# Optimization experiments

Hardware: AMD Instinct MI355X
Metric: run time of the kernel (lower is better)

The kernel has to match this reference:

```python
import jax, jax.numpy as jnp
import numpy as np

G = 8          # group (window) size -> N = G*G = 64
HEADS = 8
DIM = 256
HEAD_DIM = DIM // HEADS
SCALE = HEAD_DIM ** -0.5
POS_DIM = (DIM // 4) // 4  # 16
LN_EPS = 1e-5


def _make_bias_tables():
    # biases: coordinates (1-g..g-1) x (1-g..g-1) -> [(2g-1)^2, 2] float
    r = np.arange(1 - G, G)
    bh, bw = np.meshgrid(r, r, indexing='ij')
    biases = np.stack([bh.ravel(), bw.ravel()], axis=1).astype(np.float32)
    # relative position index [g^2, g^2]
    ch, cw = np.meshgrid(np.arange(G), np.arange(G), indexing='ij')
    coords = np.stack([ch.ravel(), cw.ravel()])              # [2, g^2]
    rel = coords[:, :, None] - coords[:, None, :]            # [2, g^2, g^2]
    rel = rel.transpose(1, 2, 0)
    rel[:, :, 0] += G - 1
    rel[:, :, 1] += G - 1
    rel[:, :, 0] *= 2 * G - 1
    rel_idx = rel.sum(-1).astype(np.int32)                   # [g^2, g^2]
    return biases, rel_idx


def setup_inputs() -> dict:
    key = jax.random.key(0)
    ks = jax.random.split(key, 8)
    B, N, C = 2048, G * G, DIM
    biases_np, rel_idx_np = _make_bias_tables()
    s = lambda fan: 1.0 / np.sqrt(fan)
    return {
        'x': jax.random.normal(ks[0], (B, N, C), jnp.float32),
        'qkv_w': jax.random.normal(ks[1], (C, 3 * C), jnp.float32) * s(C),
        'qkv_b': jnp.zeros((3 * C,), jnp.float32),
        'proj_w': jax.random.normal(ks[2], (C, C), jnp.float32) * s(C),
        'proj_b': jnp.zeros((C,), jnp.float32),
        'pos_proj_w': jax.random.normal(ks[3], (2, POS_DIM), jnp.float32) * s(2),
        'pos_proj_b': jnp.zeros((POS_DIM,), jnp.float32),
        'ln1_g': jnp.ones((POS_DIM,), jnp.float32), 'ln1_b': jnp.zeros((POS_DIM,), jnp.float32),
        'fc1_w': jax.random.normal(ks[4], (POS_DIM, POS_DIM), jnp.float32) * s(POS_DIM),
        'fc1_b': jnp.zeros((POS_DIM,), jnp.float32),
        'ln2_g': jnp.ones((POS_DIM,), jnp.float32), 'ln2_b': jnp.zeros((POS_DIM,), jnp.float32),
        'fc2_w': jax.random.normal(ks[5], (POS_DIM, POS_DIM), jnp.float32) * s(POS_DIM),
        'fc2_b': jnp.zeros((POS_DIM,), jnp.float32),
        'ln3_g': jnp.ones((POS_DIM,), jnp.float32), 'ln3_b': jnp.zeros((POS_DIM,), jnp.float32),
        'fc3_w': jax.random.normal(ks[6], (POS_DIM, HEADS), jnp.float32) * s(POS_DIM),
        'fc3_b': jnp.zeros((HEADS,), jnp.float32),
        'biases': jnp.asarray(biases_np),
        'rel_idx': jnp.asarray(rel_idx_np),
    }


def _ln(h, g, b):
    m = jnp.mean(h, -1, keepdims=True)
    v = jnp.mean((h - m) ** 2, -1, keepdims=True)
    return (h - m) * jax.lax.rsqrt(v + LN_EPS) * g + b


def reference(x, qkv_w, qkv_b, proj_w, proj_b,
              pos_proj_w, pos_proj_b,
              ln1_g, ln1_b, fc1_w, fc1_b,
              ln2_g, ln2_b, fc2_w, fc2_b,
              ln3_g, ln3_b, fc3_w, fc3_b,
              biases, rel_idx):
    B, N, C = x.shape
    # dynamic position bias MLP: [(2g-1)^2, 2] -> [(2g-1)^2, heads]
    h = biases @ pos_proj_w + pos_proj_b
    h = jax.nn.relu(_ln(h, ln1_g, ln1_b)) @ fc1_w + fc1_b
    h = jax.nn.relu(_ln(h, ln2_g, ln2_b)) @ fc2_w + fc2_b
    pos = jax.nn.relu(_ln(h, ln3_g, ln3_b)) @ fc3_w + fc3_b        # [225, H]
    rel_bias = pos[rel_idx]                                        # [N, N, H]
    rel_bias = jnp.transpose(rel_bias, (2, 0, 1))                  # [H, N, N]

    qkv = (x @ qkv_w + qkv_b).reshape(B, N, 3, HEADS, HEAD_DIM)
    qkv = jnp.transpose(qkv, (2, 0, 3, 1, 4))                      # [3, B, H, N, Dh]
    q, k, v = qkv[0] * SCALE, qkv[1], qkv[2]
    attn = jnp.einsum('bhnd,bhmd->bhnm', q, k) + rel_bias[None]    # [B, H, N, N]
    attn = jax.nn.softmax(attn, axis=-1)
    out = jnp.einsum('bhnm,bhmd->bhnd', attn, v)                   # [B, H, N, Dh]
    out = jnp.transpose(out, (0, 2, 1, 3)).reshape(B, N, C)
    return out @ proj_w + proj_b
```

## Files before the change

kernel.cpp:

```cpp
#include <hip/hip_runtime.h>

typedef _Float16 half_t;
typedef __attribute__((ext_vector_type(8))) _Float16 half8;
typedef __attribute__((ext_vector_type(4))) _Float16 half4;
typedef __attribute__((ext_vector_type(4))) float float4v;

#define LN_EPS 1e-5f
#define QK_SCALE 0.17677669529663687f

static __device__ __forceinline__ float4v mfma16(half8 a, half8 b, float4v c) {
    return __builtin_amdgcn_mfma_f32_16x16x32_f16(a, b, c, 0, 0, 0);
}

static __device__ __forceinline__ int swzA(int row, int colByte) {
    return row * 512 + ((((colByte >> 4) ^ ((row >> 1) & 7)) << 4) | (colByte & 15));
}
static __device__ __forceinline__ int swzB(int row, int colByte) {
    return row * 64 + ((((colByte >> 4) ^ ((row >> 1) & 3)) << 4) | (colByte & 15));
}

static __device__ void ln_relu16(float* h, const float* __restrict__ g, const float* __restrict__ b) {
    float m = 0.f;
    for (int j = 0; j < 16; ++j) m += h[j];
    m *= (1.0f / 16.0f);
    float v = 0.f;
    for (int j = 0; j < 16; ++j) { float d = h[j] - m; v += d * d; }
    v *= (1.0f / 16.0f);
    float rs = rsqrtf(v + LN_EPS);
    for (int j = 0; j < 16; ++j) {
        float t = (h[j] - m) * rs * g[j] + b[j];
        h[j] = t > 0.f ? t : 0.f;
    }
}

__global__ void prep_kernel(
    const float* __restrict__ qkv_w,
    const float* __restrict__ proj_w,
    const float* __restrict__ biases,
    const float* __restrict__ pos_w, const float* __restrict__ pos_b,
    const float* __restrict__ ln1_g, const float* __restrict__ ln1_b,
    const float* __restrict__ fc1_w, const float* __restrict__ fc1_b,
    const float* __restrict__ ln2_g, const float* __restrict__ ln2_b,
    const float* __restrict__ fc2_w, const float* __restrict__ fc2_b,
    const float* __restrict__ ln3_g, const float* __restrict__ ln3_b,
    const float* __restrict__ fc3_w, const float* __restrict__ fc3_b,
    const int* __restrict__ rel_idx,
    half_t* __restrict__ wqkvT,
    half_t* __restrict__ wprojT,
    float* __restrict__ rbp)
{
    __shared__ float tile[64][65];
    __shared__ float pos_s[225][8];
    const int t = blockIdx.x;
    const int tid = threadIdx.x;

    if (t < 64) {
        const float* src; half_t* dst; int ncols, rg, cg;
        if (t < 48) { src = qkv_w;  dst = wqkvT;  ncols = 768; rg = t / 12;      cg = t % 12; }
        else        { src = proj_w; dst = wprojT; ncols = 256; rg = (t-48) >> 2; cg = (t-48) & 3; }
        const int r0 = tid >> 6, c = tid & 63;
        for (int i = 0; i < 16; ++i) {
            int r = i * 4 + r0;
            tile[r][c] = src[(rg * 64 + r) * ncols + cg * 64 + c];
        }
        __syncthreads();
        for (int i = 0; i < 16; ++i) {
            int r = i * 4 + r0;
            dst[(cg * 64 + r) * 256 + rg * 64 + c] = (half_t)tile[c][r];
        }
    } else {
        if (tid < 225) {
            float h[16], h2[16];
            float b0 = biases[tid * 2], b1 = biases[tid * 2 + 1];
            for (int j = 0; j < 16; ++j) h[j] = b0 * pos_w[j] + b1 * pos_w[16 + j] + pos_b[j];
            ln_relu16(h, ln1_g, ln1_b);
            for (int j = 0; j < 16; ++j) {
                float s = fc1_b[j];
                for (int k = 0; k < 16; ++k) s += h[k] * fc1_w[k * 16 + j];
                h2[j] = s;
            }
            ln_relu16(h2, ln2_g, ln2_b);
            for (int j = 0; j < 16; ++j) {
                float s = fc2_b[j];
                for (int k = 0; k < 16; ++k) s += h2[k] * fc2_w[k * 16 + j];
                h[j] = s;
            }
            ln_relu16(h, ln3_g, ln3_b);
            for (int j = 0; j < 8; ++j) {
                float s = fc3_b[j];
                for (int k = 0; k < 16; ++k) s += h[k] * fc3_w[k * 8 + j];
                pos_s[tid][j] = s;
            }
        }
        __syncthreads();
        for (int e = tid; e < 8 * 64 * 64; e += 256) {
            int hh = e >> 12, rem = e & 4095;
            int row = rem >> 6, c = rem & 63;
            int tj = c >> 4, mm = c & 15;
            rbp[hh * 4096 + row * 64 + mm * 4 + tj] = pos_s[rel_idx[row * 64 + c]][hh];
        }
    }
}

__global__ __launch_bounds__(512, 2) void fused_kernel(
    const float* __restrict__ x,
    const half_t* __restrict__ wqkvT,
    const float* __restrict__ qkv_b,
    const half_t* __restrict__ wprojT,
    const float* __restrict__ proj_b,
    const float* __restrict__ rbp,
    float* __restrict__ out)
{
    __shared__ __align__(16) char smem[81920];
    char* xs  = smem;
    char* atn = smem;
    char* arenas = smem + 32768;

    const int b   = blockIdx.x;
    const int tid = threadIdx.x;
    const int w    = tid >> 6;
    const int lane = tid & 63;
    const int m = lane & 15;
    const int g = lane >> 4;
    char* wA = arenas + w * 6144;
    char* wB = arenas + w * 6144 + 4096;

    const float* xg = x + (size_t)b * 16384;
    #pragma unroll
    for (int i = 0; i < 8; ++i) {
        int u = tid + i * 512;
        int row = u >> 6, c4 = u & 63;
        float4v xv = *(const float4v*)(xg + u * 4);
        half4 hv;
        hv[0] = (half_t)xv[0]; hv[1] = (half_t)xv[1];
        hv[2] = (half_t)xv[2]; hv[3] = (half_t)xv[3];
        *(half4*)(xs + swzA(row, c4 * 8)) = hv;
    }
    __syncthreads();

    half8 aq[4], bk[4];
    #pragma unroll
    for (int pt = 0; pt < 2; ++pt) {
        const int wrow0 = pt * 256 + w * 32;
        #pragma unroll
        for (int c2 = 0; c2 < 2; ++c2) {
            float4v a4[4];
            #pragma unroll
            for (int ti = 0; ti < 4; ++ti) a4[ti] = {0.f, 0.f, 0.f, 0.f};
            #pragma unroll
            for (int kk = 0; kk < 8; ++kk) {
                half8 wf = *(const half8*)(wqkvT + (size_t)(wrow0 + c2 * 16 + m) * 256 + kk * 32 + g * 8);
                #pragma unroll
                for (int ti = 0; ti < 4; ++ti) {
                    half8 af = *(const half8*)(xs + swzA(ti * 16 + m, kk * 64 + g * 16));
                    a4[ti] = mfma16(wf, af, a4[ti]);
                }
            }
            float4v b4 = *(const float4v*)(qkv_b + wrow0 + c2 * 16 + g * 4);
            #pragma unroll
            for (int ti = 0; ti < 4; ++ti) {
                half4 t;
                #pragma unroll
                for (int r = 0; r < 4; ++r) t[r] = (half_t)(a4[ti][r] + b4[r]);
                *(half4*)(wA + ti * 1024 + swzB(m, (c2 * 16 + g * 4) * 2)) = t;
            }
        }
        #pragma unroll
        for (int ti = 0; ti < 4; ++ti) {
            half8 fr = *(const half8*)(wA + ti * 1024 + swzB(m, g * 16));
            if (pt == 0) aq[ti] = fr; else bk[ti] = fr;
        }
        __builtin_amdgcn_sched_barrier(0);
    }

    half4 ph[4][4];
    const float* rbh = rbp + w * 4096;
    #pragma unroll
    for (int ti = 0; ti < 4; ++ti) {
        float4v z = {0.f, 0.f, 0.f, 0.f};
        float4v s0 = mfma16(aq[ti], bk[0], z);
        float4v s1 = mfma16(aq[ti], bk[1], z);
        float4v s2 = mfma16(aq[ti], bk[2], z);
        float4v s3 = mfma16(aq[ti], bk[3], z);
        #pragma unroll
        for (int r = 0; r < 4; ++r) {
            float4v rb = *(const float4v*)(rbh + (ti * 16 + g * 4 + r) * 64 + m * 4);
            float e0 = __expf(s0[r] * QK_SCALE + rb[0]);
            float e1 = __expf(s1[r] * QK_SCALE + rb[1]);
            float e2 = __expf(s2[r] * QK_SCALE + rb[2]);
            float e3 = __expf(s3[r] * QK_SCALE + rb[3]);
            float s = e0 + e1 + e2 + e3;
            s += __shfl_xor(s, 1); s += __shfl_xor(s, 2);
            s += __shfl_xor(s, 4); s += __shfl_xor(s, 8);
            float is = 1.0f / s;
            ph[ti][0][r] = (half_t)(e0 * is);
            ph[ti][1][r] = (half_t)(e1 * is);
            ph[ti][2][r] = (half_t)(e2 * is);
            ph[ti][3][r] = (half_t)(e3 * is);
        }
    }

    half4 vh[2][4];
    #pragma unroll
    for (int c2 = 0; c2 < 2; ++c2) {
        const int wrow0 = 512 + w * 32;
        float4v a4[4];
        #pragma unroll
        for (int ti = 0; ti < 4; ++ti) a4[ti] = {0.f, 0.f, 0.f, 0.f};
        #pragma unroll
        for (int kk = 0; kk < 8; ++kk) {
            half8 wf = *(const half8*)(wqkvT + (size_t)(wrow0 + c2 * 16 + m) * 256 + kk * 32 + g * 8);
            #pragma unroll
            for (int ti = 0; ti < 4; ++ti) {
                half8 af = *(const half8*)(xs + swzA(ti * 16 + m, kk * 64 + g * 16));
                a4[ti] = mfma16(af, wf, a4[ti]);
            }
        }
        float vb = qkv_b[wrow0 + c2 * 16 + m];
        #pragma unroll
        for (int ti = 0; ti < 4; ++ti)
            #pragma unroll
            for (int r = 0; r < 4; ++r)
                vh[c2][ti][r] = (half_t)(a4[ti][r] + vb);
    }
    __syncthreads();

    #pragma unroll
    for (int tjd = 0; tjd < 2; ++tjd) {
        float4v o4[4];
        #pragma unroll
        for (int ti = 0; ti < 4; ++ti) o4[ti] = {0.f, 0.f, 0.f, 0.f};
        #pragma unroll
        for (int nc = 0; nc < 2; ++nc) {
            #pragma unroll
            for (int ti = 0; ti < 4; ++ti)
                #pragma unroll
                for (int t2 = 0; t2 < 2; ++t2)
                    #pragma unroll
                    for (int r = 0; r < 4; ++r)
                        *(half_t*)(wA + swzB(ti * 16 + g * 4 + r, (t2 * 16 + m) * 2)) =
                            ph[ti][nc * 2 + t2][r];
            #pragma unroll
            for (int t2 = 0; t2 < 2; ++t2)
                *(half4*)(wB + swzB(m, (t2 * 16 + g * 4) * 2)) = vh[tjd][nc * 2 + t2];
            half8 bv = *(const half8*)(wB + swzB(m, g * 16));
            #pragma unroll
            for (int ti = 0; ti < 4; ++ti) {
                half8 pa = *(const half8*)(wA + swzB(ti * 16 + m, g * 16));
                o4[ti] = mfma16(pa, bv, o4[ti]);
            }
            __builtin_amdgcn_sched_barrier(0);
        }
        #pragma unroll
        for (int ti = 0; ti < 4; ++ti)
            #pragma unroll
            for (int r = 0; r < 4; ++r)
                *(half_t*)(atn + swzA(ti * 16 + g * 4 + r, (w * 32 + tjd * 16 + m) * 2)) =
                    (half_t)o4[ti][r];
    }
    __syncthreads();

    float* og = out + (size_t)b * 16384;
    const int oc0 = w * 32;
    float4v pacc[2][4];
    #pragma unroll
    for (int c2 = 0; c2 < 2; ++c2)
        #pragma unroll
        for (int ti = 0; ti < 4; ++ti) pacc[c2][ti] = {0.f, 0.f, 0.f, 0.f};
    #pragma unroll
    for (int kk = 0; kk < 8; ++kk) {
        half8 wf0 = *(const half8*)(wprojT + (size_t)(oc0 +      m) * 256 + kk * 32 + g * 8);
        half8 wf1 = *(const half8*)(wprojT + (size_t)(oc0 + 16 + m) * 256 + kk * 32 + g * 8);
        #pragma unroll
        for (int ti = 0; ti < 4; ++ti) {
            half8 af = *(const half8*)(atn + swzA(ti * 16 + m, kk * 64 + g * 16));
            pacc[0][ti] = mfma16(af, wf0, pacc[0][ti]);
            pacc[1][ti] = mfma16(af, wf1, pacc[1][ti]);
        }
    }
    float pb0 = proj_b[oc0 + m], pb1 = proj_b[oc0 + 16 + m];
    #pragma unroll
    for (int c2 = 0; c2 < 2; ++c2)
        #pragma unroll
        for (int ti = 0; ti < 4; ++ti)
            #pragma unroll
            for (int r = 0; r < 4; ++r)
                og[(ti * 16 + g * 4 + r) * 256 + oc0 + c2 * 16 + m] =
                    pacc[c2][ti][r] + (c2 ? pb1 : pb0);
}

extern "C" void kernel_launch(void* const* d_in, const int* in_sizes, int n_in,
                              void* d_out, int out_size, void* d_ws, size_t ws_size,
                              hipStream_t stream) {
    const float* x          = (const float*)d_in[0];
    const float* qkv_w      = (const float*)d_in[1];
    const float* qkv_b      = (const float*)d_in[2];
    const float* proj_w     = (const float*)d_in[3];
    const float* proj_b     = (const float*)d_in[4];
    const float* pos_proj_w = (const float*)d_in[5];
    const float* pos_proj_b = (const float*)d_in[6];
    const float* ln1_g = (const float*)d_in[7];
    const float* ln1_b = (const float*)d_in[8];
    const float* fc1_w = (const float*)d_in[9];
    const float* fc1_b = (const float*)d_in[10];
    const float* ln2_g = (const float*)d_in[11];
    const float* ln2_b = (const float*)d_in[12];
    const float* fc2_w = (const float*)d_in[13];
    const float* fc2_b = (const float*)d_in[14];
    const float* ln3_g = (const float*)d_in[15];
    const float* ln3_b = (const float*)d_in[16];
    const float* fc3_w = (const float*)d_in[17];
    const float* fc3_b = (const float*)d_in[18];
    const float* biases = (const float*)d_in[19];
    const int*  rel_idx = (const int*)d_in[20];

    half_t* wqkvT  = (half_t*)d_ws;
    half_t* wprojT = (half_t*)((char*)d_ws + 393216);
    float*  rbp    = (float*)((char*)d_ws + 524288);

    const int B = in_sizes[0] / (64 * 256);

    prep_kernel<<<65, 256, 0, stream>>>(qkv_w, proj_w, biases, pos_proj_w, pos_proj_b,
                                        ln1_g, ln1_b, fc1_w, fc1_b,
                                        ln2_g, ln2_b, fc2_w, fc2_b,
                                        ln3_g, ln3_b, fc3_w, fc3_b,
                                        rel_idx, wqkvT, wprojT, rbp);
    fused_kernel<<<B, 512, 0, stream>>>(x, wqkvT, qkv_b, wprojT, proj_b, rbp,
                                        (float*)d_out);
}
```

Baseline: 258.1 us.

## Recompute softmax probabilities per chunk to cut registers and LDS for higher occupancy

Instead of holding the normalized fp16 probabilities for all 64 columns in registers, the kernel keeps only the per-row reciprocal sums and recomputes the QK scores and exponentials chunk by chunk just before the PV MMA. V is now staged once per warp in the freed x-tile region with a new swizzle, so the per-warp arena shrinks and total LDS drops from 80KB to 64KB. Launch bounds go from 2 to 4 blocks per SM, and the projection loop is split so fewer accumulators are live at once. The cost is redundant QK MFMAs, a second pass of exps and bias loads, and an extra block barrier.

```diff
diff --git a/kernel.cpp b/kernel.cpp
--- a/kernel.cpp
+++ b/kernel.cpp
@@ -17,6 +17,9 @@
 }
 static __device__ __forceinline__ int swzB(int row, int colByte) {
     return row * 64 + ((((colByte >> 4) ^ ((row >> 1) & 3)) << 4) | (colByte & 15));
+}
+static __device__ __forceinline__ int swzC(int row, int colByte) {
+    return row * 128 + ((((colByte >> 4) ^ (row & 7)) << 4) | (colByte & 15));
 }
 
 static __device__ void ln_relu16(float* h, const float* __restrict__ g, const float* __restrict__ b) {
@@ -102,7 +105,7 @@
     }
 }
 
-__global__ __launch_bounds__(512, 2) void fused_kernel(
+__global__ __launch_bounds__(512, 4) void fused_kernel(
     const float* __restrict__ x,
     const half_t* __restrict__ wqkvT,
     const float* __restrict__ qkv_b,
@@ -111,7 +114,7 @@
     const float* __restrict__ rbp,
     float* __restrict__ out)
 {
-    __shared__ __align__(16) char smem[81920];
+    __shared__ __align__(16) char smem[65536];
     char* xs  = smem;
     char* atn = smem;
     char* arenas = smem + 32768;
@@ -122,8 +125,8 @@
     const int lane = tid & 63;
     const int m = lane & 15;
     const int g = lane >> 4;
-    char* wA = arenas + w * 6144;
-    char* wB = arenas + w * 6144 + 4096;
+    char* wA  = arenas + w * 4096;
+    char* vts = xs + w * 4096;
 
     const float* xg = x + (size_t)b * 16384;
     #pragma unroll
@@ -173,7 +176,7 @@
         __builtin_amdgcn_sched_barrier(0);
     }
 
-    half4 ph[4][4];
+    float rinv[4][4];
     const float* rbh = rbp + w * 4096;
     #pragma unroll
     for (int ti = 0; ti < 4; ++ti) {
@@ -192,11 +195,7 @@
             float s = e0 + e1 + e2 + e3;
             s += __shfl_xor(s, 1); s += __shfl_xor(s, 2);
             s += __shfl_xor(s, 4); s += __shfl_xor(s, 8);
-            float is = 1.0f / s;
-            ph[ti][0][r] = (half_t)(e0 * is);
-            ph[ti][1][r] = (half_t)(e1 * is);
-            ph[ti][2][r] = (half_t)(e2 * is);
-            ph[ti][3][r] = (half_t)(e3 * is);
+            rinv[ti][r] = 1.0f / s;
         }
     }
 
@@ -226,67 +225,79 @@
     __syncthreads();
 
     #pragma unroll
-    for (int tjd = 0; tjd < 2; ++tjd) {
-        float4v o4[4];
-        #pragma unroll
-        for (int ti = 0; ti < 4; ++ti) o4[ti] = {0.f, 0.f, 0.f, 0.f};
-        #pragma unroll
-        for (int nc = 0; nc < 2; ++nc) {
-            #pragma unroll
-            for (int ti = 0; ti < 4; ++ti)
-                #pragma unroll
-                for (int t2 = 0; t2 < 2; ++t2)
-                    #pragma unroll
-                    for (int r = 0; r < 4; ++r)
-                        *(half_t*)(wA + swzB(ti * 16 + g * 4 + r, (t2 * 16 + m) * 2)) =
-                            ph[ti][nc * 2 + t2][r];
-            #pragma unroll
-            for (int t2 = 0; t2 < 2; ++t2)
-                *(half4*)(wB + swzB(m, (t2 * 16 + g * 4) * 2)) = vh[tjd][nc * 2 + t2];
-            half8 bv = *(const half8*)(wB + swzB(m, g * 16));
+    for (int c2 = 0; c2 < 2; ++c2)
+        #pragma unroll
+        for (int ti = 0; ti < 4; ++ti)
+            *(half4*)(vts + swzC(c2 * 16 + m, ti * 32 + g * 8)) = vh[c2][ti];
+
+    float4v oacc[2][4];
+    #pragma unroll
+    for (int tjd = 0; tjd < 2; ++tjd)
+        #pragma unroll
+        for (int ti = 0; ti < 4; ++ti) oacc[tjd][ti] = {0.f, 0.f, 0.f, 0.f};
+    #pragma unroll
+    for (int nc = 0; nc < 2; ++nc) {
+        #pragma unroll
+        for (int ti = 0; ti < 4; ++ti) {
+            float4v z = {0.f, 0.f, 0.f, 0.f};
+            float4v sa = mfma16(aq[ti], bk[2 * nc], z);
+            float4v sb = mfma16(aq[ti], bk[2 * nc + 1], z);
+            #pragma unroll
+            for (int r = 0; r < 4; ++r) {
+                int row = ti * 16 + g * 4 + r;
+                float4v rb = *(const float4v*)(rbh + row * 64 + m * 4);
+                float pa_ = __expf(sa[r] * QK_SCALE + rb[2 * nc])     * rinv[ti][r];
+                float pb_ = __expf(sb[r] * QK_SCALE + rb[2 * nc + 1]) * rinv[ti][r];
+                *(half_t*)(wA + swzB(row, m * 2))      = (half_t)pa_;
+                *(half_t*)(wA + swzB(row, 32 + m * 2)) = (half_t)pb_;
+            }
+        }
+        #pragma unroll
+        for (int tjd = 0; tjd < 2; ++tjd) {
+            half8 bv = *(const half8*)(vts + swzC(tjd * 16 + m, nc * 64 + g * 16));
             #pragma unroll
             for (int ti = 0; ti < 4; ++ti) {
                 half8 pa = *(const half8*)(wA + swzB(ti * 16 + m, g * 16));
-                o4[ti] = mfma16(pa, bv, o4[ti]);
-            }
-            __builtin_amdgcn_sched_barrier(0);
-        }
+                oacc[tjd][ti] = mfma16(pa, bv, oacc[tjd][ti]);
+            }
+        }
+        __builtin_amdgcn_sched_barrier(0);
+    }
+    __syncthreads();
+
+    #pragma unroll
+    for (int tjd = 0; tjd < 2; ++tjd)
         #pragma unroll
         for (int ti = 0; ti < 4; ++ti)
             #pragma unroll
             for (int r = 0; r < 4; ++r)
                 *(half_t*)(atn + swzA(ti * 16 + g * 4 + r, (w * 32 + tjd * 16 + m) * 2)) =
-                    (half_t)o4[ti][r];
-    }
+                    (half_t)oacc[tjd][ti][r];
     __syncthreads();
 
     float* og = out + (size_t)b * 16384;
     const int oc0 = w * 32;
-    float4v pacc[2][4];
-    #pragma unroll
-    for (int c2 = 0; c2 < 2; ++c2)
-        #pragma unroll
-        for (int ti = 0; ti < 4; ++ti) pacc[c2][ti] = {0.f, 0.f, 0.f, 0.f};
-    #pragma unroll
-    for (int kk = 0; kk < 8; ++kk) {
-        half8 wf0 = *(const half8*)(wprojT + (size_t)(oc0 +      m) * 256 + kk * 32 + g * 8);
-        half8 wf1 = *(const half8*)(wprojT + (size_t)(oc0 + 16 + m) * 256 + kk * 32 + g * 8);
-        #pragma unroll
-        for (int ti = 0; ti < 4; ++ti) {
-            half8 af = *(const half8*)(atn + swzA(ti * 16 + m, kk * 64 + g * 16));
-            pacc[0][ti] = mfma16(af, wf0, pacc[0][ti]);
-            pacc[1][ti] = mfma16(af, wf1, pacc[1][ti]);
-        }
-    }
-    float pb0 = proj_b[oc0 + m], pb1 = proj_b[oc0 + 16 + m];
-    #pragma unroll
-    for (int c2 = 0; c2 < 2; ++c2)
+    #pragma unroll
+    for (int c2 = 0; c2 < 2; ++c2) {
+        float4v p4[4];
+        #pragma unroll
+        for (int ti = 0; ti < 4; ++ti) p4[ti] = {0.f, 0.f, 0.f, 0.f};
+        #pragma unroll
+        for (int kk = 0; kk < 8; ++kk) {
+            half8 wf = *(const half8*)(wprojT + (size_t)(oc0 + c2 * 16 + m) * 256 + kk * 32 + g * 8);
+            #pragma unroll
+            for (int ti = 0; ti < 4; ++ti) {
+                half8 af = *(const half8*)(atn + swzA(ti * 16 + m, kk * 64 + g * 16));
+                p4[ti] = mfma16(af, wf, p4[ti]);
+            }
+        }
+        float pb = proj_b[oc0 + c2 * 16 + m];
         #pragma unroll
         for (int ti = 0; ti < 4; ++ti)
             #pragma unroll
             for (int r = 0; r < 4; ++r)
-                og[(ti * 16 + g * 4 + r) * 256 + oc0 + c2 * 16 + m] =
-                    pacc[c2][ti][r] + (c2 ? pb1 : pb0);
+                og[(ti * 16 + g * 4 + r) * 256 + oc0 + c2 * 16 + m] = p4[ti][r] + pb;
+    }
 }
 
 extern "C" void kernel_launch(void* const* d_in, const int* in_sizes, int n_in,
```

After: 581.3 us. +125.2%, slower.

## Halve block to 4 waves, each processing two heads, shrink LDS arenas

Applied to the files above, without the earlier changes.

The fused attention kernel now launches 256 threads per window, and each wave handles two heads in sequence instead of one. Per-wave LDS scratch shrinks, so total shared memory per block drops from 80KB to 52KB, allowing more blocks per CU (launch bounds changed to 256,3). The PV stage is reordered so P fragments are loaded once and reused across both V column tiles, and the projection loop now runs four 16-column tiles per wave. Per-head outputs are held in registers across the loop, which raises register pressure. There is also less intra-block parallelism per window.

```diff
diff --git a/kernel.cpp b/kernel.cpp
--- a/kernel.cpp
+++ b/kernel.cpp
@@ -102,7 +102,7 @@
     }
 }
 
-__global__ __launch_bounds__(512, 2) void fused_kernel(
+__global__ __launch_bounds__(256, 3) void fused_kernel(
     const float* __restrict__ x,
     const half_t* __restrict__ wqkvT,
     const float* __restrict__ qkv_b,
@@ -111,10 +111,9 @@
     const float* __restrict__ rbp,
     float* __restrict__ out)
 {
-    __shared__ __align__(16) char smem[81920];
+    __shared__ __align__(16) char smem[53248];
     char* xs  = smem;
     char* atn = smem;
-    char* arenas = smem + 32768;
 
     const int b   = blockIdx.x;
     const int tid = threadIdx.x;
@@ -122,13 +121,13 @@
     const int lane = tid & 63;
     const int m = lane & 15;
     const int g = lane >> 4;
-    char* wA = arenas + w * 6144;
-    char* wB = arenas + w * 6144 + 4096;
+    char* wA = smem + 32768 + w * 5120;
+    char* wB = wA + 4096;
 
     const float* xg = x + (size_t)b * 16384;
     #pragma unroll
-    for (int i = 0; i < 8; ++i) {
-        int u = tid + i * 512;
+    for (int i = 0; i < 16; ++i) {
+        int u = tid + i * 256;
         int row = u >> 6, c4 = u & 63;
         float4v xv = *(const float4v*)(xg + u * 4);
         half4 hv;
@@ -138,12 +137,78 @@
     }
     __syncthreads();
 
-    half8 aq[4], bk[4];
+    half4 oh[2][2][4];
+
     #pragma unroll
-    for (int pt = 0; pt < 2; ++pt) {
-        const int wrow0 = pt * 256 + w * 32;
+    for (int hh = 0; hh < 2; ++hh) {
+        const int h = w + hh * 4;
+        const float* rbh = rbp + h * 4096;
+
+        half8 aq[4], bk[4];
+        #pragma unroll
+        for (int pt = 0; pt < 2; ++pt) {
+            const int wrow0 = pt * 256 + h * 32;
+            #pragma unroll
+            for (int c2 = 0; c2 < 2; ++c2) {
+                float4v a4[4];
+                #pragma unroll
+                for (int ti = 0; ti < 4; ++ti) a4[ti] = {0.f, 0.f, 0.f, 0.f};
+                #pragma unroll
+                for (int kk = 0; kk < 8; ++kk) {
+                    half8 wf = *(const half8*)(wqkvT + (size_t)(wrow0 + c2 * 16 + m) * 256 + kk * 32 + g * 8);
+                    #pragma unroll
+                    for (int ti = 0; ti < 4; ++ti) {
+                        half8 af = *(const half8*)(xs + swzA(ti * 16 + m, kk * 64 + g * 16));
+                        a4[ti] = mfma16(wf, af, a4[ti]);
+                    }
+                }
+                float4v b4 = *(const float4v*)(qkv_b + wrow0 + c2 * 16 + g * 4);
+                #pragma unroll
+                for (int ti = 0; ti < 4; ++ti) {
+                    half4 t;
+                    #pragma unroll
+                    for (int r = 0; r < 4; ++r) t[r] = (half_t)(a4[ti][r] + b4[r]);
+                    *(half4*)(wA + ti * 1024 + swzB(m, (c2 * 16 + g * 4) * 2)) = t;
+                }
+            }
+            #pragma unroll
+            for (int ti = 0; ti < 4; ++ti) {
+                half8 fr = *(const half8*)(wA + ti * 1024 + swzB(m, g * 16));
+                if (pt == 0) aq[ti] = fr; else bk[ti] = fr;
+            }
+            __builtin_amdgcn_sched_barrier(0);
+        }
+
+        half4 ph[4][4];
+        #pragma unroll
+        for (int ti = 0; ti < 4; ++ti) {
+            float4v z = {0.f, 0.f, 0.f, 0.f};
+            float4v s0 = mfma16(aq[ti], bk[0], z);
+            float4v s1 = mfma16(aq[ti], bk[1], z);
+            float4v s2 = mfma16(aq[ti], bk[2], z);
+            float4v s3 = mfma16(aq[ti], bk[3], z);
+            #pragma unroll
+            for (int r = 0; r < 4; ++r) {
+                float4v rb = *(const float4v*)(rbh + (ti * 16 + g * 4 + r) * 64 + m * 4);
+                float e0 = __expf(s0[r] * QK_SCALE + rb[0]);
+                float e1 = __expf(s1[r] * QK_SCALE + rb[1]);
+                float e2 = __expf(s2[r] * QK_SCALE + rb[2]);
+                float e3 = __expf(s3[r] * QK_SCALE + rb[3]);
+                float s = e0 + e1 + e2 + e3;
+                s += __shfl_xor(s, 1); s += __shfl_xor(s, 2);
+                s += __shfl_xor(s, 4); s += __shfl_xor(s, 8);
+                float is = 1.0f / s;
+                ph[ti][0][r] = (half_t)(e0 * is);
+                ph[ti][1][r] = (half_t)(e1 * is);
+                ph[ti][2][r] = (half_t)(e2 * is);
+                ph[ti][3][r] = (half_t)(e3 * is);
+            }
+        }
+
+        half4 vh[2][4];
         #pragma unroll
         for (int c2 = 0; c2 < 2; ++c2) {
+            const int wrow0 = 512 + h * 32;
             float4v a4[4];
             #pragma unroll
             for (int ti = 0; ti < 4; ++ti) a4[ti] = {0.f, 0.f, 0.f, 0.f};
@@ -153,83 +218,22 @@
                 #pragma unroll
                 for (int ti = 0; ti < 4; ++ti) {
                     half8 af = *(const half8*)(xs + swzA(ti * 16 + m, kk * 64 + g * 16));
-                    a4[ti] = mfma16(wf, af, a4[ti]);
+                    a4[ti] = mfma16(af, wf, a4[ti]);
                 }
             }
-            float4v b4 = *(const float4v*)(qkv_b + wrow0 + c2 * 16 + g * 4);
-            #pragma unroll
-            for (int ti = 0; ti < 4; ++ti) {
-                half4 t;
-                #pragma unroll
-                for (int r = 0; r < 4; ++r) t[r] = (half_t)(a4[ti][r] + b4[r]);
-                *(half4*)(wA + ti * 1024 + swzB(m, (c2 * 16 + g * 4) * 2)) = t;
-            }
-        }
-        #pragma unroll
-        for (int ti = 0; ti < 4; ++ti) {
-            half8 fr = *(const half8*)(wA + ti * 1024 + swzB(m, g * 16));
-            if (pt == 0) aq[ti] = fr; else bk[ti] = fr;
-        }
-        __builtin_amdgcn_sched_barrier(0);
-    }
-
-    half4 ph[4][4];
-    const float* rbh = rbp + w * 4096;
-    #pragma unroll
-    for (int ti = 0; ti < 4; ++ti) {
-        float4v z = {0.f, 0.f, 0.f, 0.f};
-        float4v s0 = mfma16(aq[ti], bk[0], z);
-        float4v s1 = mfma16(aq[ti], bk[1], z);
-        float4v s2 = mfma16(aq[ti], bk[2], z);
-        float4v s3 = mfma16(aq[ti], bk[3], z);
-        #pragma unroll
-        for (int r = 0; r < 4; ++r) {
-            float4v rb = *(const float4v*)(rbh + (ti * 16 + g * 4 + r) * 64 + m * 4);
-            float e0 = __expf(s0[r] * QK_SCALE + rb[0]);
-            float e1 = __expf(s1[r] * QK_SCALE + rb[1]);
-            float e2 = __expf(s2[r] * QK_SCALE + rb[2]);
-            float e3 = __expf(s3[r] * QK_SCALE + rb[3]);
-            float s = e0 + e1 + e2 + e3;
-            s += __shfl_xor(s, 1); s += __shfl_xor(s, 2);
-            s += __shfl_xor(s, 4); s += __shfl_xor(s, 8);
-            float is = 1.0f / s;
-            ph[ti][0][r] = (half_t)(e0 * is);
-            ph[ti][1][r] = (half_t)(e1 * is);
-            ph[ti][2][r] = (half_t)(e2 * is);
-            ph[ti][3][r] = (half_t)(e3 * is);
-        }
-    }
-
-    half4 vh[2][4];
-    #pragma unroll
-    for (int c2 = 0; c2 < 2; ++c2) {
-        const int wrow0 = 512 + w * 32;
-        float4v a4[4];
-        #pragma unroll
-        for (int ti = 0; ti < 4; ++ti) a4[ti] = {0.f, 0.f, 0.f, 0.f};
-        #pragma unroll
-        for (int kk = 0; kk < 8; ++kk) {
-            half8 wf = *(const half8*)(wqkvT + (size_t)(wrow0 + c2 * 16 + m) * 256 + kk * 32 + g * 8);
-            #pragma unroll
-            for (int ti = 0; ti < 4; ++ti) {
-                half8 af = *(const half8*)(xs + swzA(ti * 16 + m, kk * 64 + g * 16));
-                a4[ti] = mfma16(af, wf, a4[ti]);
-            }
-        }
-        float vb = qkv_b[wrow0 + c2 * 16 + m];
-        #pragma unroll
-        for (int ti = 0; ti < 4; ++ti)
-            #pragma unroll
-            for (int r = 0; r < 4; ++r)
-                vh[c2][ti][r] = (half_t)(a4[ti][r] + vb);
-    }
-    __syncthreads();
-
-    #pragma unroll
-    for (int tjd = 0; tjd < 2; ++tjd) {
-        float4v o4[4];
-        #pragma unroll
-        for (int ti = 0; ti < 4; ++ti) o4[ti] = {0.f, 0.f, 0.f, 0.f};
+            float vb = qkv_b[wrow0 + c2 * 16 + m];
+            #pragma unroll
+            for (int ti = 0; ti < 4; ++ti)
+                #pragma unroll
+                for (int r = 0; r < 4; ++r)
+                    vh[c2][ti][r] = (half_t)(a4[ti][r] + vb);
+        }
+
+        float4v oacc[2][4];
+        #pragma unroll
+        for (int tjd = 0; tjd < 2; ++tjd)
+            #pragma unroll
+            for (int ti = 0; ti < 4; ++ti) oacc[tjd][ti] = {0.f, 0.f, 0.f, 0.f};
         #pragma unroll
         for (int nc = 0; nc < 2; ++nc) {
             #pragma unroll
@@ -240,53 +244,70 @@
                     for (int r = 0; r < 4; ++r)
                         *(half_t*)(wA + swzB(ti * 16 + g * 4 + r, (t2 * 16 + m) * 2)) =
                             ph[ti][nc * 2 + t2][r];
-            #pragma unroll
-            for (int t2 = 0; t2 < 2; ++t2)
-                *(half4*)(wB + swzB(m, (t2 * 16 + g * 4) * 2)) = vh[tjd][nc * 2 + t2];
-            half8 bv = *(const half8*)(wB + swzB(m, g * 16));
+            half8 pa[4];
+            #pragma unroll
+            for (int ti = 0; ti < 4; ++ti)
+                pa[ti] = *(const half8*)(wA + swzB(ti * 16 + m, g * 16));
+            __builtin_amdgcn_sched_barrier(0);
+            #pragma unroll
+            for (int tjd = 0; tjd < 2; ++tjd) {
+                #pragma unroll
+                for (int t2 = 0; t2 < 2; ++t2)
+                    *(half4*)(wB + swzB(m, (t2 * 16 + g * 4) * 2)) = vh[tjd][nc * 2 + t2];
+                half8 bv = *(const half8*)(wB + swzB(m, g * 16));
+                #pragma unroll
+                for (int ti = 0; ti < 4; ++ti)
+                    oacc[tjd][ti] = mfma16(pa[ti], bv, oacc[tjd][ti]);
+                __builtin_amdgcn_sched_barrier(0);
+            }
+        }
+        #pragma unroll
+        for (int tjd = 0; tjd < 2; ++tjd)
+            #pragma unroll
+            for (int ti = 0; ti < 4; ++ti)
+                #pragma unroll
+                for (int r = 0; r < 4; ++r)
+                    oh[hh][tjd][ti][r] = (half_t)oacc[tjd][ti][r];
+        __builtin_amdgcn_sched_barrier(0);
+    }
+    __syncthreads();
+
+    #pragma unroll
+    for (int hh = 0; hh < 2; ++hh)
+        #pragma unroll
+        for (int tjd = 0; tjd < 2; ++tjd)
+            #pragma unroll
+            for (int ti = 0; ti < 4; ++ti)
+                #pragma unroll
+                for (int r = 0; r < 4; ++r)
+                    *(half_t*)(atn + swzA(ti * 16 + g * 4 + r,
+                                          ((w + hh * 4) * 32 + tjd * 16 + m) * 2)) =
+                        oh[hh][tjd][ti][r];
+    __syncthreads();
+
+    float* og = out + (size_t)b * 16384;
+    #pragma unroll
+    for (int c4 = 0; c4 < 4; ++c4) {
+        const int oc0 = w * 64 + c4 * 16;
+        float4v p4[4];
+        #pragma unroll
+        for (int ti = 0; ti < 4; ++ti) p4[ti] = {0.f, 0.f, 0.f, 0.f};
+        #pragma unroll
+        for (int kk = 0; kk < 8; ++kk) {
+            half8 wf = *(const half8*)(wprojT + (size_t)(oc0 + m) * 256 + kk * 32 + g * 8);
             #pragma unroll
             for (int ti = 0; ti < 4; ++ti) {
-                half8 pa = *(const half8*)(wA + swzB(ti * 16 + m, g * 16));
-                o4[ti] = mfma16(pa, bv, o4[ti]);
-            }
-            __builtin_amdgcn_sched_barrier(0);
-        }
+                half8 af = *(const half8*)(atn + swzA(ti * 16 + m, kk * 64 + g * 16));
+                p4[ti] = mfma16(af, wf, p4[ti]);
+            }
+        }
+        float pb = proj_b[oc0 + m];
         #pragma unroll
         for (int ti = 0; ti < 4; ++ti)
             #pragma unroll
             for (int r = 0; r < 4; ++r)
-                *(half_t*)(atn + swzA(ti * 16 + g * 4 + r, (w * 32 + tjd * 16 + m) * 2)) =
-                    (half_t)o4[ti][r];
-    }
-    __syncthreads();
-
-    float* og = out + (size_t)b * 16384;
-    const int oc0 = w * 32;
-    float4v pacc[2][4];
-    #pragma unroll
-    for (int c2 = 0; c2 < 2; ++c2)
-        #pragma unroll
-        for (int ti = 0; ti < 4; ++ti) pacc[c2][ti] = {0.f, 0.f, 0.f, 0.f};
-    #pragma unroll
-    for (int kk = 0; kk < 8; ++kk) {
-        half8 wf0 = *(const half8*)(wprojT + (size_t)(oc0 +      m) * 256 + kk * 32 + g * 8);
-        half8 wf1 = *(const half8*)(wprojT + (size_t)(oc0 + 16 + m) * 256 + kk * 32 + g * 8);
-        #pragma unroll
-        for (int ti = 0; ti < 4; ++ti) {
-            half8 af = *(const half8*)(atn + swzA(ti * 16 + m, kk * 64 + g * 16));
-            pacc[0][ti] = mfma16(af, wf0, pacc[0][ti]);
-            pacc[1][ti] = mfma16(af, wf1, pacc[1][ti]);
-        }
-    }
-    float pb0 = proj_b[oc0 + m], pb1 = proj_b[oc0 + 16 + m];
-    #pragma unroll
-    for (int c2 = 0; c2 < 2; ++c2)
-        #pragma unroll
-        for (int ti = 0; ti < 4; ++ti)
-            #pragma unroll
-            for (int r = 0; r < 4; ++r)
-                og[(ti * 16 + g * 4 + r) * 256 + oc0 + c2 * 16 + m] =
-                    pacc[c2][ti][r] + (c2 ? pb1 : pb0);
+                og[(ti * 16 + g * 4 + r) * 256 + oc0 + m] = p4[ti][r] + pb;
+    }
 }
 
 extern "C" void kernel_launch(void* const* d_in, const int* in_sizes, int n_in,
@@ -325,6 +346,6 @@
                                         ln2_g, ln2_b, fc2_w, fc2_b,
                                         ln3_g, ln3_b, fc3_w, fc3_b,
                                         rel_idx, wqkvT, wprojT, rbp);
-    fused_kernel<<<B, 512, 0, stream>>>(x, wqkvT, qkv_b, wprojT, proj_b, rbp,
+    fused_kernel<<<B, 256, 0, stream>>>(x, wqkvT, qkv_b, wprojT, proj_b, rbp,
                                         (float*)d_out);
 }
```

Result: slower. 345.3 us (+33.8%).

## Fuse Q/K projection loops, stage V in shared memory, shrink LDS footprint

Applied to the files above, without the earlier changes.

Q and K projections are computed in a single k-loop so each x fragment read from LDS feeds four MFMA accumulators, and V columns are likewise computed together. V is written once into a swizzled per-wave region that reuses the x buffer, so the PV product no longer rewrites V for each output tile. The P fragments are loaded once and reused across both output column tiles. Shared memory drops from 80KB to 64KB, which may help occupancy, at the cost of more live accumulator registers and one extra block barrier.

```diff
diff --git a/kernel.cpp b/kernel.cpp
--- a/kernel.cpp
+++ b/kernel.cpp
@@ -17,6 +17,9 @@
 }
 static __device__ __forceinline__ int swzB(int row, int colByte) {
     return row * 64 + ((((colByte >> 4) ^ ((row >> 1) & 3)) << 4) | (colByte & 15));
+}
+static __device__ __forceinline__ int swzC(int row, int colByte) {
+    return row * 128 + ((((colByte >> 4) ^ (row & 7)) << 4) | (colByte & 15));
 }
 
 static __device__ void ln_relu16(float* h, const float* __restrict__ g, const float* __restrict__ b) {
@@ -111,7 +114,7 @@
     const float* __restrict__ rbp,
     float* __restrict__ out)
 {
-    __shared__ __align__(16) char smem[81920];
+    __shared__ __align__(16) char smem[65536];
     char* xs  = smem;
     char* atn = smem;
     char* arenas = smem + 32768;
@@ -122,8 +125,8 @@
     const int lane = tid & 63;
     const int m = lane & 15;
     const int g = lane >> 4;
-    char* wA = arenas + w * 6144;
-    char* wB = arenas + w * 6144 + 4096;
+    char* wA  = arenas + w * 4096;
+    char* vts = xs + w * 4096;
 
     const float* xg = x + (size_t)b * 16384;
     #pragma unroll
@@ -138,38 +141,67 @@
     }
     __syncthreads();
 
+    float4v qb[2][2];
+    #pragma unroll
+    for (int pt = 0; pt < 2; ++pt)
+        #pragma unroll
+        for (int c2 = 0; c2 < 2; ++c2)
+            qb[pt][c2] = *(const float4v*)(qkv_b + pt * 256 + w * 32 + c2 * 16 + g * 4);
+
     half8 aq[4], bk[4];
-    #pragma unroll
-    for (int pt = 0; pt < 2; ++pt) {
-        const int wrow0 = pt * 256 + w * 32;
-        #pragma unroll
-        for (int c2 = 0; c2 < 2; ++c2) {
-            float4v a4[4];
-            #pragma unroll
-            for (int ti = 0; ti < 4; ++ti) a4[ti] = {0.f, 0.f, 0.f, 0.f};
-            #pragma unroll
-            for (int kk = 0; kk < 8; ++kk) {
-                half8 wf = *(const half8*)(wqkvT + (size_t)(wrow0 + c2 * 16 + m) * 256 + kk * 32 + g * 8);
-                #pragma unroll
-                for (int ti = 0; ti < 4; ++ti) {
-                    half8 af = *(const half8*)(xs + swzA(ti * 16 + m, kk * 64 + g * 16));
-                    a4[ti] = mfma16(wf, af, a4[ti]);
-                }
-            }
-            float4v b4 = *(const float4v*)(qkv_b + wrow0 + c2 * 16 + g * 4);
+    {
+        float4v qa[2][4], ka[2][4];
+        #pragma unroll
+        for (int c2 = 0; c2 < 2; ++c2)
+            #pragma unroll
+            for (int ti = 0; ti < 4; ++ti) {
+                qa[c2][ti] = {0.f, 0.f, 0.f, 0.f};
+                ka[c2][ti] = {0.f, 0.f, 0.f, 0.f};
+            }
+        const half_t* wqb = wqkvT + (size_t)(w * 32 + m) * 256 + g * 8;
+        #pragma unroll
+        for (int kk = 0; kk < 8; ++kk) {
+            half8 af[4];
+            #pragma unroll
+            for (int ti = 0; ti < 4; ++ti)
+                af[ti] = *(const half8*)(xs + swzA(ti * 16 + m, kk * 64 + g * 16));
+            half8 wq0 = *(const half8*)(wqb + kk * 32);
+            half8 wq1 = *(const half8*)(wqb + 16 * 256 + kk * 32);
+            half8 wk0 = *(const half8*)(wqb + 256 * 256 + kk * 32);
+            half8 wk1 = *(const half8*)(wqb + 272 * 256 + kk * 32);
+            #pragma unroll
+            for (int ti = 0; ti < 4; ++ti) {
+                qa[0][ti] = mfma16(wq0, af[ti], qa[0][ti]);
+                qa[1][ti] = mfma16(wq1, af[ti], qa[1][ti]);
+                ka[0][ti] = mfma16(wk0, af[ti], ka[0][ti]);
+                ka[1][ti] = mfma16(wk1, af[ti], ka[1][ti]);
+            }
+        }
+        #pragma unroll
+        for (int c2 = 0; c2 < 2; ++c2)
             #pragma unroll
             for (int ti = 0; ti < 4; ++ti) {
                 half4 t;
                 #pragma unroll
-                for (int r = 0; r < 4; ++r) t[r] = (half_t)(a4[ti][r] + b4[r]);
+                for (int r = 0; r < 4; ++r) t[r] = (half_t)(qa[c2][ti][r] + qb[0][c2][r]);
                 *(half4*)(wA + ti * 1024 + swzB(m, (c2 * 16 + g * 4) * 2)) = t;
             }
-        }
-        #pragma unroll
-        for (int ti = 0; ti < 4; ++ti) {
-            half8 fr = *(const half8*)(wA + ti * 1024 + swzB(m, g * 16));
-            if (pt == 0) aq[ti] = fr; else bk[ti] = fr;
-        }
+        #pragma unroll
+        for (int ti = 0; ti < 4; ++ti)
+            aq[ti] = *(const half8*)(wA + ti * 1024 + swzB(m, g * 16));
+        __builtin_amdgcn_sched_barrier(0);
+        #pragma unroll
+        for (int c2 = 0; c2 < 2; ++c2)
+            #pragma unroll
+            for (int ti = 0; ti < 4; ++ti) {
+                half4 t;
+                #pragma unroll
+                for (int r = 0; r < 4; ++r) t[r] = (half_t)(ka[c2][ti][r] + qb[1][c2][r]);
+                *(half4*)(wA + ti * 1024 + swzB(m, (c2 * 16 + g * 4) * 2)) = t;
+            }
+        #pragma unroll
+        for (int ti = 0; ti < 4; ++ti)
+            bk[ti] = *(const half8*)(wA + ti * 1024 + swzB(m, g * 16));
         __builtin_amdgcn_sched_barrier(0);
     }
 
@@ -201,63 +233,79 @@
     }
 
     half4 vh[2][4];
-    #pragma unroll
-    for (int c2 = 0; c2 < 2; ++c2) {
-        const int wrow0 = 512 + w * 32;
-        float4v a4[4];
-        #pragma unroll
-        for (int ti = 0; ti < 4; ++ti) a4[ti] = {0.f, 0.f, 0.f, 0.f};
+    {
+        float4v va[2][4];
+        #pragma unroll
+        for (int c2 = 0; c2 < 2; ++c2)
+            #pragma unroll
+            for (int ti = 0; ti < 4; ++ti) va[c2][ti] = {0.f, 0.f, 0.f, 0.f};
+        const half_t* wvb = wqkvT + (size_t)(512 + w * 32 + m) * 256 + g * 8;
         #pragma unroll
         for (int kk = 0; kk < 8; ++kk) {
-            half8 wf = *(const half8*)(wqkvT + (size_t)(wrow0 + c2 * 16 + m) * 256 + kk * 32 + g * 8);
+            half8 wv0 = *(const half8*)(wvb + kk * 32);
+            half8 wv1 = *(const half8*)(wvb + 16 * 256 + kk * 32);
             #pragma unroll
             for (int ti = 0; ti < 4; ++ti) {
                 half8 af = *(const half8*)(xs + swzA(ti * 16 + m, kk * 64 + g * 16));
-                a4[ti] = mfma16(af, wf, a4[ti]);
-            }
-        }
-        float vb = qkv_b[wrow0 + c2 * 16 + m];
-        #pragma unroll
-        for (int ti = 0; ti < 4; ++ti)
-            #pragma unroll
-            for (int r = 0; r < 4; ++r)
-                vh[c2][ti][r] = (half_t)(a4[ti][r] + vb);
-    }
-    __syncthreads();
-
-    #pragma unroll
-    for (int tjd = 0; tjd < 2; ++tjd) {
-        float4v o4[4];
-        #pragma unroll
-        for (int ti = 0; ti < 4; ++ti) o4[ti] = {0.f, 0.f, 0.f, 0.f};
-        #pragma unroll
-        for (int nc = 0; nc < 2; ++nc) {
+                va[0][ti] = mfma16(af, wv0, va[0][ti]);
+                va[1][ti] = mfma16(af, wv1, va[1][ti]);
+            }
+        }
+        float vb0 = qkv_b[512 + w * 32 + m], vb1 = qkv_b[512 + w * 32 + 16 + m];
+        #pragma unroll
+        for (int c2 = 0; c2 < 2; ++c2)
             #pragma unroll
             for (int ti = 0; ti < 4; ++ti)
                 #pragma unroll
-                for (int t2 = 0; t2 < 2; ++t2)
-                    #pragma unroll
-                    for (int r = 0; r < 4; ++r)
-                        *(half_t*)(wA + swzB(ti * 16 + g * 4 + r, (t2 * 16 + m) * 2)) =
-                            ph[ti][nc * 2 + t2][r];
+                for (int r = 0; r < 4; ++r)
+                    vh[c2][ti][r] = (half_t)(va[c2][ti][r] + (c2 ? vb1 : vb0));
+    }
+    __syncthreads();
+
+    #pragma unroll
+    for (int c2 = 0; c2 < 2; ++c2)
+        #pragma unroll
+        for (int ti = 0; ti < 4; ++ti)
+            *(half4*)(vts + swzC(c2 * 16 + m, ti * 32 + g * 8)) = vh[c2][ti];
+
+    float4v oacc[2][4];
+    #pragma unroll
+    for (int tjd = 0; tjd < 2; ++tjd)
+        #pragma unroll
+        for (int ti = 0; ti < 4; ++ti) oacc[tjd][ti] = {0.f, 0.f, 0.f, 0.f};
+    #pragma unroll
+    for (int nc = 0; nc < 2; ++nc) {
+        #pragma unroll
+        for (int ti = 0; ti < 4; ++ti)
             #pragma unroll
             for (int t2 = 0; t2 < 2; ++t2)
-                *(half4*)(wB + swzB(m, (t2 * 16 + g * 4) * 2)) = vh[tjd][nc * 2 + t2];
-            half8 bv = *(const half8*)(wB + swzB(m, g * 16));
-            #pragma unroll
-            for (int ti = 0; ti < 4; ++ti) {
-                half8 pa = *(const half8*)(wA + swzB(ti * 16 + m, g * 16));
-                o4[ti] = mfma16(pa, bv, o4[ti]);
-            }
-            __builtin_amdgcn_sched_barrier(0);
-        }
+                #pragma unroll
+                for (int r = 0; r < 4; ++r)
+                    *(half_t*)(wA + swzB(ti * 16 + g * 4 + r, (t2 * 16 + m) * 2)) =
+                        ph[ti][nc * 2 + t2][r];
+        half8 pa[4];
+        #pragma unroll
+        for (int ti = 0; ti < 4; ++ti)
+            pa[ti] = *(const half8*)(wA + swzB(ti * 16 + m, g * 16));
+        #pragma unroll
+        for (int tjd = 0; tjd < 2; ++tjd) {
+            half8 bv = *(const half8*)(vts + swzC(tjd * 16 + m, nc * 64 + g * 16));
+            #pragma unroll
+            for (int ti = 0; ti < 4; ++ti)
+                oacc[tjd][ti] = mfma16(pa[ti], bv, oacc[tjd][ti]);
+        }
+        __builtin_amdgcn_sched_barrier(0);
+    }
+    __syncthreads();
+
+    #pragma unroll
+    for (int tjd = 0; tjd < 2; ++tjd)
         #pragma unroll
         for (int ti = 0; ti < 4; ++ti)
             #pragma unroll
             for (int r = 0; r < 4; ++r)
                 *(half_t*)(atn + swzA(ti * 16 + g * 4 + r, (w * 32 + tjd * 16 + m) * 2)) =
-                    (half_t)o4[ti][r];
-    }
+                    (half_t)oacc[tjd][ti][r];
     __syncthreads();
 
     float* og = out + (size_t)b * 16384;
@@ -267,10 +315,11 @@
     for (int c2 = 0; c2 < 2; ++c2)
         #pragma unroll
         for (int ti = 0; ti < 4; ++ti) pacc[c2][ti] = {0.f, 0.f, 0.f, 0.f};
+    const half_t* wpb = wprojT + (size_t)(oc0 + m) * 256 + g * 8;
     #pragma unroll
     for (int kk = 0; kk < 8; ++kk) {
-        half8 wf0 = *(const half8*)(wprojT + (size_t)(oc0 +      m) * 256 + kk * 32 + g * 8);
-        half8 wf1 = *(const half8*)(wprojT + (size_t)(oc0 + 16 + m) * 256 + kk * 32 + g * 8);
+        half8 wf0 = *(const half8*)(wpb + kk * 32);
+        half8 wf1 = *(const half8*)(wpb + 16 * 256 + kk * 32);
         #pragma unroll
         for (int ti = 0; ti < 4; ++ti) {
             half8 af = *(const half8*)(atn + swzA(ti * 16 + m, kk * 64 + g * 16));
```

After: 264.2 us. 1.02x slower.
